# Performance work log

Hardware: AMD Instinct MI355X
Metric: run time of the kernel (lower is better)

Reference implementation:

```python
import jax, jax.numpy as jnp
import numpy as np

B, S, H, E, V = 128, 128, 1024, 512, 32000

def setup_inputs() -> dict:
    key = jax.random.key(0)
    ks = jax.random.split(key, 14)
    sc = 0.02
    return {
        "x": jax.random.randint(ks[0], (B,), 0, V),
        "hidden": jax.random.normal(ks[1], (1, B, H), jnp.float32),
        "cell": jax.random.normal(ks[2], (1, B, H), jnp.float32),
        "encoder_outputs": jax.random.normal(ks[3], (B, S, H), jnp.float32),
        # parameters
        "emb_table": jax.random.normal(ks[4], (V, E), jnp.float32) * sc,
        "attn_W": jax.random.normal(ks[5], (H, 2 * H), jnp.float32) * sc,
        "attn_b": jnp.zeros((H,), jnp.float32),
        "v": jax.random.uniform(ks[6], (H,), jnp.float32),
        "W_ih": jax.random.normal(ks[7], (4 * H, E + H), jnp.float32) * sc,
        "W_hh": jax.random.normal(ks[8], (4 * H, H), jnp.float32) * sc,
        "b_ih": jnp.zeros((4 * H,), jnp.float32),
        "b_hh": jnp.zeros((4 * H,), jnp.float32),
        "fc_W": jax.random.normal(ks[9], (V, 2 * H), jnp.float32) * sc,
        "fc_b": jnp.zeros((V,), jnp.float32),
    }


def reference(x, hidden, cell, encoder_outputs, emb_table, attn_W, attn_b, v,
              W_ih, W_hh, b_ih, b_hh, fc_W, fc_b):
    b, s, h = encoder_outputs.shape
    h_last = hidden[-1]                      # [B,H]
    c_last = cell[-1]                        # [B,H]

    # Bahdanau attention
    h_rep = jnp.broadcast_to(h_last[:, None, :], (b, s, h))          # [B,S,H]
    cat = jnp.concatenate([h_rep, encoder_outputs], axis=2)          # [B,S,2H]
    energy = jnp.tanh(jnp.einsum('bsk,hk->bsh', cat, attn_W) + attn_b)
    score = jnp.einsum('bsh,h->bs', energy, v)                       # [B,S]
    attn_weights = jax.nn.softmax(score, axis=1)                     # [B,S]
    context = jnp.einsum('bs,bsh->bh', attn_weights, encoder_outputs)  # [B,H]

    # LSTM single step, gate order i,f,g,o (PyTorch convention)
    emb = emb_table[x]                                               # [B,E]
    xin = jnp.concatenate([emb, context], axis=1)                    # [B,E+H]
    gates = xin @ W_ih.T + b_ih + h_last @ W_hh.T + b_hh             # [B,4H]
    i, f, g, o = jnp.split(gates, 4, axis=1)
    c_new = jax.nn.sigmoid(f) * c_last + jax.nn.sigmoid(i) * jnp.tanh(g)
    h_new = jax.nn.sigmoid(o) * jnp.tanh(c_new)

    out = jnp.concatenate([h_new, context], axis=1)                  # [B,2H]
    logits = out @ fc_W.T + fc_b                                     # [B,V]
    return logits, h_new[None], c_new[None], attn_weights
```

## Files before the change

kernel.cpp:

```cpp
#include <hip/hip_runtime.h>
#include <hip/hip_bf16.h>
#include <math.h>

constexpr int B  = 128;
constexpr int S  = 128;
constexpr int H  = 1024;
constexpr int E  = 512;
constexpr int V  = 32000;
constexpr int H2 = 2 * H;
constexpr int G4 = 4 * H;
constexpr int KX = E + H;
constexpr int KG = KX + H;
constexpr int BS = B * S;
constexpr int KSPLIT = 4;
constexpr int KSEG = KG / KSPLIT;

typedef float  f32x4  __attribute__((ext_vector_type(4)));
typedef short  short8 __attribute__((ext_vector_type(8)));

__device__ __forceinline__ short f2bf(float f) {
    union { float f; unsigned u; } x; x.f = f;
    unsigned r = (x.u + 0x7FFFu + ((x.u >> 16) & 1u)) >> 16;
    return (short)r;
}
__device__ __forceinline__ float bf2f(unsigned short u) {
    union { unsigned u; float f; } x; x.u = ((unsigned)u) << 16;
    return x.f;
}
__device__ __forceinline__ float fast_tanh(float x) {
    float z = fminf(fmaxf(x, -15.f), 15.f);
    float e = __expf(2.f * z);
    return 1.f - __fdividef(2.f, e + 1.f);
}
__device__ __forceinline__ short8 cvt8(float4 a, float4 b) {
    short8 r;
    r[0] = f2bf(a.x); r[1] = f2bf(a.y); r[2] = f2bf(a.z); r[3] = f2bf(a.w);
    r[4] = f2bf(b.x); r[5] = f2bf(b.y); r[6] = f2bf(b.z); r[7] = f2bf(b.w);
    return r;
}
__device__ __forceinline__ void glds16(const void* g, void* l) {
    __builtin_amdgcn_global_load_lds(
        (const __attribute__((address_space(1))) unsigned int*)g,
        (__attribute__((address_space(3))) unsigned int*)l,
        16, 0, 0);
}

__global__ __launch_bounds__(256) void k_pre(const float* __restrict__ enc,
                                             short* __restrict__ encb,
                                             const float* __restrict__ attn_W,
                                             short* __restrict__ w2b,
                                             const float* __restrict__ hlast,
                                             const float* __restrict__ attn_b,
                                             float* __restrict__ q) {
    int bid = blockIdx.x;
    if (bid < 512) {
        int idx = bid * 256 + threadIdx.x;
        int b = idx >> 10;
        int h = idx & (H - 1);
        const float* arow = attn_W + (size_t)h * H2;
        const float* hrow = hlast + (size_t)b * H;
        float acc = 0.f;
        for (int k = 0; k < H; k += 4) {
            float4 a = *(const float4*)(arow + k);
            float4 x = *(const float4*)(hrow + k);
            acc += a.x * x.x + a.y * x.y + a.z * x.z + a.w * x.w;
        }
        q[idx] = acc + attn_b[h];
    } else if (bid < 512 + 16384) {
        size_t p = (size_t)(bid - 512) * 256 + threadIdx.x;
        float4 a = *(const float4*)(enc + p * 4);
        short4 o = { f2bf(a.x), f2bf(a.y), f2bf(a.z), f2bf(a.w) };
        *(short4*)(encb + p * 4) = o;
    } else {
        int p = (bid - 16896) * 256 + threadIdx.x;
        int row = p >> 8;
        int c = (p & 255) * 4;
        float4 a = *(const float4*)(attn_W + (size_t)row * H2 + H + c);
        short4 o = { f2bf(a.x), f2bf(a.y), f2bf(a.z), f2bf(a.w) };
        *(short4*)(w2b + (size_t)row * H + c) = o;
    }
}

__global__ __launch_bounds__(256) void k_energy_mfma(const short* __restrict__ encb,
                                                     const short* __restrict__ w2b,
                                                     const float* __restrict__ q,
                                                     const float* __restrict__ v,
                                                     float* __restrict__ part) {
    __shared__ __align__(16) char smem[32768];
    short* Af = (short*)smem;
    short* Bf = (short*)(smem + 16384);
    float (*red)[33] = (float(*)[33])smem;

    const int tid  = threadIdx.x;
    const int wave = tid >> 6, lane = tid & 63;
    const int wr = wave >> 1, wc = wave & 1;
    const int c16 = lane & 15, q4 = lane >> 4;
    const int m0 = blockIdx.x * 128;
    const int n0 = blockIdx.y * 128;

    f32x4 acc[4][4] = {};

    const int scA   = ((lane & 3) ^ ((lane >> 3) & 3)) * 8;
    const int rowA0 = wave * 32 + (lane >> 2);
    const int rowA1 = rowA0 + 16;
    const int sa    = (c16 >> 1) & 3;

    const short* gA = encb + (size_t)m0 * H;
    const short* gB = w2b + (size_t)n0 * H;

    auto stage = [&](int k0, int dst) {
        glds16(gA + (size_t)rowA0 * H + k0 + scA, Af + dst + wave * 1024);
        glds16(gA + (size_t)rowA1 * H + k0 + scA, Af + dst + wave * 1024 + 512);
        glds16(gB + (size_t)rowA0 * H + k0 + scA, Bf + dst + wave * 1024);
        glds16(gB + (size_t)rowA1 * H + k0 + scA, Bf + dst + wave * 1024 + 512);
    };

    stage(0, 0);
    __syncthreads();

    for (int kk = 0; kk < 32; kk++) {
        const int bo = (kk & 1) << 12;
        if (kk < 31) stage((kk + 1) * 32, bo ^ 4096);

        short8 a[4], b[4];
#pragma unroll
        for (int i = 0; i < 4; i++) {
            int r = wr * 64 + i * 16 + c16;
            a[i] = *(const short8*)(Af + bo + r * 32 + (q4 ^ sa) * 8);
        }
#pragma unroll
        for (int j = 0; j < 4; j++) {
            int r = wc * 64 + j * 16 + c16;
            b[j] = *(const short8*)(Bf + bo + r * 32 + (q4 ^ sa) * 8);
        }
#pragma unroll
        for (int i = 0; i < 4; i++)
#pragma unroll
            for (int j = 0; j < 4; j++)
                acc[i][j] = __builtin_amdgcn_mfma_f32_16x16x32_bf16(a[i], b[j], acc[i][j], 0, 0, 0);

        if (kk < 31) __syncthreads();
    }
    __syncthreads();

    const float* qb = q + (size_t)blockIdx.x * H;
#pragma unroll
    for (int i = 0; i < 4; i++) {
#pragma unroll
        for (int r = 0; r < 4; r++) {
            float s = 0.f;
#pragma unroll
            for (int j = 0; j < 4; j++) {
                int n = n0 + wc * 64 + j * 16 + c16;
                s += v[n] * fast_tanh(qb[n] + acc[i][j][r]);
            }
            red[wr * 64 + i * 16 + q4 * 4 + r][wc * 16 + c16] = s;
        }
    }
    __syncthreads();
    if (tid < 128) {
        float s = 0.f;
#pragma unroll
        for (int c = 0; c < 32; c++) s += red[tid][c];
        part[(size_t)(m0 + tid) * 8 + blockIdx.y] = s;
    }
}

__global__ __launch_bounds__(256) void k_softmax_ctx(const float* __restrict__ part,
                                                     const short* __restrict__ encb,
                                                     const int* __restrict__ x,
                                                     const float* __restrict__ emb,
                                                     const float* __restrict__ hlast,
                                                     float* __restrict__ attn_out,
                                                     short* __restrict__ xinb) {
    const int bid = blockIdx.x;
    const int b = bid >> 2, ch = bid & 3;
    const int tid = threadIdx.x;
    __shared__ float w[S];
    __shared__ float red[128];

    float val = 0.f;
    if (tid < S) {
        const float* p = part + (size_t)(b * S + tid) * 8;
#pragma unroll
        for (int t = 0; t < 8; t++) val += p[t];
        w[tid] = val;
        red[tid] = val;
    }
    __syncthreads();
#pragma unroll
    for (int s = 64; s > 0; s >>= 1) {
        if (tid < s) red[tid] = fmaxf(red[tid], red[tid + s]);
        __syncthreads();
    }
    float m = red[0];
    __syncthreads();
    if (tid < S) { val = __expf(w[tid] - m); red[tid] = val; }
    __syncthreads();
#pragma unroll
    for (int s = 64; s > 0; s >>= 1) {
        if (tid < s) red[tid] += red[tid + s];
        __syncthreads();
    }
    float inv = 1.f / red[0];
    if (tid < S) {
        val *= inv;
        w[tid] = val;
        if (ch == 0) attn_out[b * S + tid] = val;
    }
    if (ch == 1) {
        int xv = x[b];
        float2 e2 = *(const float2*)(emb + (size_t)xv * E + tid * 2);
        short2 eo = { f2bf(e2.x), f2bf(e2.y) };
        *(short2*)(xinb + (size_t)b * KG + tid * 2) = eo;
    } else if (ch == 2) {
        float4 h4 = *(const float4*)(hlast + (size_t)b * H + tid * 4);
        short4 ho = { f2bf(h4.x), f2bf(h4.y), f2bf(h4.z), f2bf(h4.w) };
        *(short4*)(xinb + (size_t)b * KG + KX + tid * 4) = ho;
    }
    __syncthreads();

    const int h = ch * 256 + tid;
    const unsigned short* e = (const unsigned short*)encb + (size_t)b * S * H + h;
    float a0 = 0.f;
#pragma unroll 8
    for (int s = 0; s < S; s++) a0 += w[s] * bf2f(e[(size_t)s * H]);
    xinb[(size_t)b * KG + E + h] = f2bf(a0);
}

__global__ __launch_bounds__(256) void k_gates_mfma(const short* __restrict__ xinb,
                                                    const float* __restrict__ W_ih,
                                                    const float* __restrict__ W_hh,
                                                    float* __restrict__ gpart) {
    __shared__ __align__(16) short A_s[2 * 4096];
    __shared__ __align__(16) float B_s[2 * 1024];

    const int tid  = threadIdx.x;
    const int wave = tid >> 6, lane = tid & 63;
    const int c16 = lane & 15, q4 = lane >> 4;
    const int n0 = blockIdx.x * 32;
    const int kbeg = blockIdx.y * KSEG;

    const int scA   = ((lane & 3) ^ ((lane >> 3) & 3)) * 8;
    const int rowA0 = wave * 32 + (lane >> 2);
    const int rowA1 = rowA0 + 16;
    const int rowB  = wave * 8 + (lane >> 3);
    const int scB   = ((lane & 7) ^ ((lane >> 3) & 7)) * 4;
    const int sa = (c16 >> 1) & 3;
    const int sb = c16 & 7;

    const short* gA0 = xinb + (size_t)rowA0 * KG + scA;
    const short* gA1 = xinb + (size_t)rowA1 * KG + scA;
    const int nr = n0 + rowB;

    auto bsrc = [&](int k0) -> const float* {
        return (k0 < KX) ? (W_ih + (size_t)nr * KX + k0 + scB)
                         : (W_hh + (size_t)nr * H + (k0 - KX) + scB);
    };
    auto stage = [&](int k0, int abo, int bbo) {
        glds16(gA0 + k0, A_s + abo + wave * 1024);
        glds16(gA1 + k0, A_s + abo + wave * 1024 + 512);
        glds16(bsrc(k0), B_s + bbo + wave * 256);
    };

    f32x4 acc[2][2] = {};
    stage(kbeg, 0, 0);
    __syncthreads();

    for (int kk = 0; kk < KSEG / 32; kk++) {
        const int abo = (kk & 1) << 12;
        const int bbo = (kk & 1) << 10;
        if (kk < KSEG / 32 - 1) stage(kbeg + (kk + 1) * 32, abo ^ 4096, bbo ^ 1024);

        short8 a[2], bfr[2];
#pragma unroll
        for (int i = 0; i < 2; i++) {
            int r = wave * 32 + i * 16 + c16;
            a[i] = *(const short8*)(A_s + abo + r * 32 + (q4 ^ sa) * 8);
        }
#pragma unroll
        for (int j = 0; j < 2; j++) {
            int rb = j * 16 + c16;
            int cl = (2 * q4) ^ sb;
            float4 lo = *(const float4*)(B_s + bbo + rb * 32 + cl * 4);
            float4 hi = *(const float4*)(B_s + bbo + rb * 32 + (cl ^ 1) * 4);
            bfr[j] = cvt8(lo, hi);
        }
#pragma unroll
        for (int i = 0; i < 2; i++)
#pragma unroll
            for (int j = 0; j < 2; j++)
                acc[i][j] = __builtin_amdgcn_mfma_f32_16x16x32_bf16(a[i], bfr[j], acc[i][j], 0, 0, 0);

        if (kk < KSEG / 32 - 1) __syncthreads();
    }

    float* gp = gpart + (size_t)blockIdx.y * B * G4;
#pragma unroll
    for (int i = 0; i < 2; i++)
#pragma unroll
        for (int j = 0; j < 2; j++)
#pragma unroll
            for (int r = 0; r < 4; r++) {
                int R = wave * 32 + i * 16 + q4 * 4 + r;
                int n = n0 + j * 16 + c16;
                gp[(size_t)R * G4 + n] = acc[i][j][r];
            }
}

__global__ __launch_bounds__(256) void k_lstm(const float* __restrict__ gpart,
                                              const float* __restrict__ cell,
                                              const float* __restrict__ b_ih,
                                              const float* __restrict__ b_hh,
                                              const short* __restrict__ xinb,
                                              float* __restrict__ out_h,
                                              float* __restrict__ out_c,
                                              short* __restrict__ xoutb) {
    int idx = blockIdx.x * 256 + threadIdx.x;
    int b = idx >> 10;
    int h = idx & (H - 1);
    float ig = b_ih[h]         + b_hh[h];
    float fg = b_ih[H + h]     + b_hh[H + h];
    float gg = b_ih[2 * H + h] + b_hh[2 * H + h];
    float og = b_ih[3 * H + h] + b_hh[3 * H + h];
#pragma unroll
    for (int p = 0; p < KSPLIT; p++) {
        const float* g = gpart + ((size_t)p * B + b) * G4;
        ig += g[h]; fg += g[H + h]; gg += g[2 * H + h]; og += g[3 * H + h];
    }
    float si = 1.f / (1.f + expf(-ig));
    float sf = 1.f / (1.f + expf(-fg));
    float so = 1.f / (1.f + expf(-og));
    float c = sf * cell[idx] + si * tanhf(gg);
    float hn = so * tanhf(c);
    out_h[idx] = hn;
    out_c[idx] = c;
    xoutb[(size_t)b * H2 + h] = f2bf(hn);
    xoutb[(size_t)b * H2 + H + h] = xinb[(size_t)b * KG + E + h];
}

__global__ __launch_bounds__(256) void k_fc_mfma(const short* __restrict__ xoutb,
                                                 const float* __restrict__ fcW,
                                                 const float* __restrict__ fcb,
                                                 float* __restrict__ logits) {
    __shared__ __align__(16) short A_s[2 * 4096];
    __shared__ __align__(16) float B_s[2 * 1024];

    const int tid  = threadIdx.x;
    const int wave = tid >> 6, lane = tid & 63;
    const int c16 = lane & 15, q4 = lane >> 4;
    const int n0 = blockIdx.x * 32;

    const int scA   = ((lane & 3) ^ ((lane >> 3) & 3)) * 8;
    const int rowA0 = wave * 32 + (lane >> 2);
    const int rowA1 = rowA0 + 16;
    const int rowB  = wave * 8 + (lane >> 3);
    const int scB   = ((lane & 7) ^ ((lane >> 3) & 7)) * 4;
    const int sa = (c16 >> 1) & 3;
    const int sb = c16 & 7;

    const short* gA0 = xoutb + (size_t)rowA0 * H2 + scA;
    const short* gA1 = xoutb + (size_t)rowA1 * H2 + scA;
    const float* gBr = fcW + (size_t)(n0 + rowB) * H2 + scB;

    auto stage = [&](int k0, int abo, int bbo) {
        glds16(gA0 + k0, A_s + abo + wave * 1024);
        glds16(gA1 + k0, A_s + abo + wave * 1024 + 512);
        glds16(gBr + k0, B_s + bbo + wave * 256);
    };

    f32x4 acc[2][2] = {};
    stage(0, 0, 0);
    __syncthreads();

    for (int kk = 0; kk < H2 / 32; kk++) {
        const int abo = (kk & 1) << 12;
        const int bbo = (kk & 1) << 10;
        if (kk < H2 / 32 - 1) stage((kk + 1) * 32, abo ^ 4096, bbo ^ 1024);

        short8 a[2], bfr[2];
#pragma unroll
        for (int i = 0; i < 2; i++) {
            int r = wave * 32 + i * 16 + c16;
            a[i] = *(const short8*)(A_s + abo + r * 32 + (q4 ^ sa) * 8);
        }
#pragma unroll
        for (int j = 0; j < 2; j++) {
            int rb = j * 16 + c16;
            int cl = (2 * q4) ^ sb;
            float4 lo = *(const float4*)(B_s + bbo + rb * 32 + cl * 4);
            float4 hi = *(const float4*)(B_s + bbo + rb * 32 + (cl ^ 1) * 4);
            bfr[j] = cvt8(lo, hi);
        }
#pragma unroll
        for (int i = 0; i < 2; i++)
#pragma unroll
            for (int j = 0; j < 2; j++)
                acc[i][j] = __builtin_amdgcn_mfma_f32_16x16x32_bf16(a[i], bfr[j], acc[i][j], 0, 0, 0);

        if (kk < H2 / 32 - 1) __syncthreads();
    }

#pragma unroll
    for (int i = 0; i < 2; i++)
#pragma unroll
        for (int j = 0; j < 2; j++) {
            int n = n0 + j * 16 + c16;
            float bias = fcb[n];
#pragma unroll
            for (int r = 0; r < 4; r++) {
                int R = wave * 32 + i * 16 + q4 * 4 + r;
                logits[(size_t)R * V + n] = acc[i][j][r] + bias;
            }
        }
}

extern "C" void kernel_launch(void* const* d_in, const int* in_sizes, int n_in,
                              void* d_out, int out_size, void* d_ws, size_t ws_size,
                              hipStream_t stream) {
    const int*   x      = (const int*)d_in[0];
    const float* hidden = (const float*)d_in[1];
    const float* cell   = (const float*)d_in[2];
    const float* enc    = (const float*)d_in[3];
    const float* emb    = (const float*)d_in[4];
    const float* attn_W = (const float*)d_in[5];
    const float* attn_b = (const float*)d_in[6];
    const float* v      = (const float*)d_in[7];
    const float* W_ih   = (const float*)d_in[8];
    const float* W_hh   = (const float*)d_in[9];
    const float* b_ih   = (const float*)d_in[10];
    const float* b_hh   = (const float*)d_in[11];
    const float* fc_W   = (const float*)d_in[12];
    const float* fc_b   = (const float*)d_in[13];

    float* out = (float*)d_out;
    float* logits   = out;
    float* out_h    = out + (size_t)B * V;
    float* out_c    = out_h + (size_t)B * H;
    float* out_attn = out_c + (size_t)B * H;

    char* ws = (char*)d_ws;
    short* encb  = (short*)ws;   ws += (size_t)BS * H * 2;
    short* w2b   = (short*)ws;   ws += (size_t)H * H * 2;
    short* xinb  = (short*)ws;   ws += (size_t)B * KG * 2;
    short* xoutb = (short*)ws;   ws += (size_t)B * H2 * 2;
    float* q     = (float*)ws;   ws += (size_t)B * H * 4;
    float* part  = (float*)ws;   ws += (size_t)BS * 8 * 4;
    float* gpart = (float*)ws;   ws += (size_t)KSPLIT * B * G4 * 4;

    k_pre<<<dim3(512 + 16384 + 1024), dim3(256), 0, stream>>>(enc, encb, attn_W, w2b,
                                                              hidden, attn_b, q);
    k_energy_mfma<<<dim3(BS / 128, H / 128), dim3(256), 0, stream>>>(encb, w2b, q, v, part);
    k_softmax_ctx<<<dim3(B * 4), dim3(256), 0, stream>>>(part, encb, x, emb, hidden, out_attn, xinb);
    k_gates_mfma<<<dim3(G4 / 32, KSPLIT), dim3(256), 0, stream>>>(xinb, W_ih, W_hh, gpart);
    k_lstm<<<dim3(B * H / 256), dim3(256), 0, stream>>>(gpart, cell, b_ih, b_hh, xinb,
                                                        out_h, out_c, xoutb);
    k_fc_mfma<<<dim3(V / 32), dim3(256), 0, stream>>>(xoutb, fc_W, fc_b, logits);
}
```

Measured before the change: 640.9 us.

## Move query projection to split-K MFMA kernel and streamline GEMM barriers

Moves the h_last·attn_W query projection out of the scalar FP32 loop inside k_pre into a new split-K bf16 MFMA kernel. Its partial sums are reduced and the bias is added in the energy kernel's epilogue, which now also keeps q and v in registers. All MFMA GEMM loops replace __syncthreads with an explicit vmcnt wait, sched_barrier and s_barrier, so the prefetch of the next stage can stay in flight across the barrier. The query now uses bf16 inputs, which adds rounding error, and the hand-counted vmcnt values must match the number of loads issued per stage.

Result: faster. 580.9 us (-9.4%).

```diff
diff --git a/kernel.cpp b/kernel.cpp
--- a/kernel.cpp
+++ b/kernel.cpp
@@ -14,9 +14,15 @@
 constexpr int BS = B * S;
 constexpr int KSPLIT = 4;
 constexpr int KSEG = KG / KSPLIT;
+constexpr int QSPLIT = 4;
+constexpr int QSEG = H / QSPLIT;
 
 typedef float  f32x4  __attribute__((ext_vector_type(4)));
 typedef short  short8 __attribute__((ext_vector_type(8)));
+
+#define VMCNT(N) asm volatile("s_waitcnt vmcnt(" #N ")" ::: "memory")
+#define SBAR     asm volatile("s_barrier" ::: "memory")
+#define SCHED0   __builtin_amdgcn_sched_barrier(0)
 
 __device__ __forceinline__ short f2bf(float f) {
     union { float f; unsigned u; } x; x.f = f;
@@ -48,31 +54,15 @@
 __global__ __launch_bounds__(256) void k_pre(const float* __restrict__ enc,
                                              short* __restrict__ encb,
                                              const float* __restrict__ attn_W,
-                                             short* __restrict__ w2b,
-                                             const float* __restrict__ hlast,
-                                             const float* __restrict__ attn_b,
-                                             float* __restrict__ q) {
+                                             short* __restrict__ w2b) {
     int bid = blockIdx.x;
-    if (bid < 512) {
-        int idx = bid * 256 + threadIdx.x;
-        int b = idx >> 10;
-        int h = idx & (H - 1);
-        const float* arow = attn_W + (size_t)h * H2;
-        const float* hrow = hlast + (size_t)b * H;
-        float acc = 0.f;
-        for (int k = 0; k < H; k += 4) {
-            float4 a = *(const float4*)(arow + k);
-            float4 x = *(const float4*)(hrow + k);
-            acc += a.x * x.x + a.y * x.y + a.z * x.z + a.w * x.w;
-        }
-        q[idx] = acc + attn_b[h];
-    } else if (bid < 512 + 16384) {
-        size_t p = (size_t)(bid - 512) * 256 + threadIdx.x;
+    if (bid < 16384) {
+        size_t p = (size_t)bid * 256 + threadIdx.x;
         float4 a = *(const float4*)(enc + p * 4);
         short4 o = { f2bf(a.x), f2bf(a.y), f2bf(a.z), f2bf(a.w) };
         *(short4*)(encb + p * 4) = o;
     } else {
-        int p = (bid - 16896) * 256 + threadIdx.x;
+        int p = (bid - 16384) * 256 + threadIdx.x;
         int row = p >> 8;
         int c = (p & 255) * 4;
         float4 a = *(const float4*)(attn_W + (size_t)row * H2 + H + c);
@@ -81,9 +71,91 @@
     }
 }
 
+__global__ __launch_bounds__(256) void k_q_mfma(const float* __restrict__ hlast,
+                                                const float* __restrict__ attn_W,
+                                                float* __restrict__ qpart) {
+    __shared__ __align__(16) float A_s[2 * 4096];
+    __shared__ __align__(16) float B_s[2 * 1024];
+
+    const int tid  = threadIdx.x;
+    const int wave = tid >> 6, lane = tid & 63;
+    const int c16 = lane & 15, q4 = lane >> 4;
+    const int n0 = blockIdx.x * 32;
+    const int kbeg = blockIdx.y * QSEG;
+
+    const int sc = ((lane & 7) ^ ((lane >> 3) & 7)) * 4;
+    const int rA = (lane >> 3);
+    const int rowB = wave * 8 + (lane >> 3);
+
+    const float* gB = attn_W + (size_t)(n0 + rowB) * H2 + sc;
+
+    auto stage = [&](int k0, int abo, int bbo) {
+#pragma unroll
+        for (int j = 0; j < 4; j++) {
+            int row = wave * 32 + j * 8 + rA;
+            glds16(hlast + (size_t)row * H + k0 + sc,
+                   A_s + abo + wave * 1024 + j * 256);
+        }
+        glds16(gB + k0, B_s + bbo + wave * 256);
+    };
+
+    f32x4 acc[2][2] = {};
+    stage(kbeg, 0, 0);
+
+    for (int kk = 0; kk < QSEG / 32; kk++) {
+        const int abo = (kk & 1) << 12;
+        const int bbo = (kk & 1) << 10;
+        if (kk < QSEG / 32 - 1) {
+            stage(kbeg + (kk + 1) * 32, abo ^ 4096, bbo ^ 1024);
+            VMCNT(5);
+        } else {
+            VMCNT(0);
+        }
+        SCHED0; SBAR;
+
+        short8 a[2], bfr[2];
+#pragma unroll
+        for (int i = 0; i < 2; i++) {
+            int ar = wave * 32 + i * 16 + c16;
+            int cl = (2 * q4) ^ (ar & 7);
+            float4 lo = *(const float4*)(A_s + abo + ar * 32 + cl * 4);
+            float4 hi = *(const float4*)(A_s + abo + ar * 32 + (cl ^ 1) * 4);
+            a[i] = cvt8(lo, hi);
+        }
+#pragma unroll
+        for (int j = 0; j < 2; j++) {
+            int rb = j * 16 + c16;
+            int cl = (2 * q4) ^ (rb & 7);
+            float4 lo = *(const float4*)(B_s + bbo + rb * 32 + cl * 4);
+            float4 hi = *(const float4*)(B_s + bbo + rb * 32 + (cl ^ 1) * 4);
+            bfr[j] = cvt8(lo, hi);
+        }
+#pragma unroll
+        for (int i = 0; i < 2; i++)
+#pragma unroll
+            for (int j = 0; j < 2; j++)
+                acc[i][j] = __builtin_amdgcn_mfma_f32_16x16x32_bf16(a[i], bfr[j], acc[i][j], 0, 0, 0);
+
+        SCHED0; SBAR;
+    }
+
+    float* qp = qpart + (size_t)blockIdx.y * B * H;
+#pragma unroll
+    for (int i = 0; i < 2; i++)
+#pragma unroll
+        for (int j = 0; j < 2; j++)
+#pragma unroll
+            for (int r = 0; r < 4; r++) {
+                int R = wave * 32 + i * 16 + q4 * 4 + r;
+                int n = n0 + j * 16 + c16;
+                qp[(size_t)R * H + n] = acc[i][j][r];
+            }
+}
+
 __global__ __launch_bounds__(256) void k_energy_mfma(const short* __restrict__ encb,
                                                      const short* __restrict__ w2b,
-                                                     const float* __restrict__ q,
+                                                     const float* __restrict__ qpart,
+                                                     const float* __restrict__ attn_b,
                                                      const float* __restrict__ v,
                                                      float* __restrict__ part) {
     __shared__ __align__(16) char smem[32768];
@@ -116,11 +188,16 @@
     };
 
     stage(0, 0);
-    __syncthreads();
 
     for (int kk = 0; kk < 32; kk++) {
         const int bo = (kk & 1) << 12;
-        if (kk < 31) stage((kk + 1) * 32, bo ^ 4096);
+        if (kk < 31) {
+            stage((kk + 1) * 32, bo ^ 4096);
+            VMCNT(4);
+        } else {
+            VMCNT(0);
+        }
+        SCHED0; SBAR;
 
         short8 a[4], b[4];
 #pragma unroll
@@ -139,21 +216,30 @@
             for (int j = 0; j < 4; j++)
                 acc[i][j] = __builtin_amdgcn_mfma_f32_16x16x32_bf16(a[i], b[j], acc[i][j], 0, 0, 0);
 
-        if (kk < 31) __syncthreads();
-    }
-    __syncthreads();
-
-    const float* qb = q + (size_t)blockIdx.x * H;
+        SCHED0; SBAR;
+    }
+
+    const int bb = blockIdx.x;
+    float qv[4], vv[4];
+#pragma unroll
+    for (int j = 0; j < 4; j++) {
+        int n = n0 + wc * 64 + j * 16 + c16;
+        float s = attn_b[n];
+#pragma unroll
+        for (int kh = 0; kh < QSPLIT; kh++)
+            s += qpart[((size_t)kh * B + bb) * H + n];
+        qv[j] = s;
+        vv[j] = v[n];
+    }
+
 #pragma unroll
     for (int i = 0; i < 4; i++) {
 #pragma unroll
         for (int r = 0; r < 4; r++) {
             float s = 0.f;
 #pragma unroll
-            for (int j = 0; j < 4; j++) {
-                int n = n0 + wc * 64 + j * 16 + c16;
-                s += v[n] * fast_tanh(qb[n] + acc[i][j][r]);
-            }
+            for (int j = 0; j < 4; j++)
+                s += vv[j] * fast_tanh(qv[j] + acc[i][j][r]);
             red[wr * 64 + i * 16 + q4 * 4 + r][wc * 16 + c16] = s;
         }
     }
@@ -265,12 +351,17 @@
 
     f32x4 acc[2][2] = {};
     stage(kbeg, 0, 0);
-    __syncthreads();
 
     for (int kk = 0; kk < KSEG / 32; kk++) {
         const int abo = (kk & 1) << 12;
         const int bbo = (kk & 1) << 10;
-        if (kk < KSEG / 32 - 1) stage(kbeg + (kk + 1) * 32, abo ^ 4096, bbo ^ 1024);
+        if (kk < KSEG / 32 - 1) {
+            stage(kbeg + (kk + 1) * 32, abo ^ 4096, bbo ^ 1024);
+            VMCNT(3);
+        } else {
+            VMCNT(0);
+        }
+        SCHED0; SBAR;
 
         short8 a[2], bfr[2];
 #pragma unroll
@@ -292,7 +383,7 @@
             for (int j = 0; j < 2; j++)
                 acc[i][j] = __builtin_amdgcn_mfma_f32_16x16x32_bf16(a[i], bfr[j], acc[i][j], 0, 0, 0);
 
-        if (kk < KSEG / 32 - 1) __syncthreads();
+        SCHED0; SBAR;
     }
 
     float* gp = gpart + (size_t)blockIdx.y * B * G4;
@@ -371,12 +462,17 @@
 
     f32x4 acc[2][2] = {};
     stage(0, 0, 0);
-    __syncthreads();
 
     for (int kk = 0; kk < H2 / 32; kk++) {
         const int abo = (kk & 1) << 12;
         const int bbo = (kk & 1) << 10;
-        if (kk < H2 / 32 - 1) stage((kk + 1) * 32, abo ^ 4096, bbo ^ 1024);
+        if (kk < H2 / 32 - 1) {
+            stage((kk + 1) * 32, abo ^ 4096, bbo ^ 1024);
+            VMCNT(3);
+        } else {
+            VMCNT(0);
+        }
+        SCHED0; SBAR;
 
         short8 a[2], bfr[2];
 #pragma unroll
@@ -398,7 +494,7 @@
             for (int j = 0; j < 2; j++)
                 acc[i][j] = __builtin_amdgcn_mfma_f32_16x16x32_bf16(a[i], bfr[j], acc[i][j], 0, 0, 0);
 
-        if (kk < H2 / 32 - 1) __syncthreads();
+        SCHED0; SBAR;
     }
 
 #pragma unroll
@@ -444,13 +540,14 @@
     short* w2b   = (short*)ws;   ws += (size_t)H * H * 2;
     short* xinb  = (short*)ws;   ws += (size_t)B * KG * 2;
     short* xoutb = (short*)ws;   ws += (size_t)B * H2 * 2;
-    float* q     = (float*)ws;   ws += (size_t)B * H * 4;
+    float* qpart = (float*)ws;   ws += (size_t)QSPLIT * B * H * 4;
     float* part  = (float*)ws;   ws += (size_t)BS * 8 * 4;
     float* gpart = (float*)ws;   ws += (size_t)KSPLIT * B * G4 * 4;
 
-    k_pre<<<dim3(512 + 16384 + 1024), dim3(256), 0, stream>>>(enc, encb, attn_W, w2b,
-                                                              hidden, attn_b, q);
-    k_energy_mfma<<<dim3(BS / 128, H / 128), dim3(256), 0, stream>>>(encb, w2b, q, v, part);
+    k_q_mfma<<<dim3(H / 32, QSPLIT), dim3(256), 0, stream>>>(hidden, attn_W, qpart);
+    k_pre<<<dim3(16384 + 1024), dim3(256), 0, stream>>>(enc, encb, attn_W, w2b);
+    k_energy_mfma<<<dim3(BS / 128, H / 128), dim3(256), 0, stream>>>(encb, w2b, qpart,
+                                                                     attn_b, v, part);
     k_softmax_ctx<<<dim3(B * 4), dim3(256), 0, stream>>>(part, encb, x, emb, hidden, out_attn, xinb);
     k_gates_mfma<<<dim3(G4 / 32, KSPLIT), dim3(256), 0, stream>>>(xinb, W_ih, W_hh, gpart);
     k_lstm<<<dim3(B * H / 256), dim3(256), 0, stream>>>(gpart, cell, b_ih, b_hh, xinb,
```
